# Optimization experiments

Hardware: AMD Instinct MI355X
Metric: run time of the kernel (lower is better)

Reference implementation:

```python
import jax, jax.numpy as jnp
import numpy as np

B, S, DM, NH, DK, DFF = 4, 2048, 512, 8, 64, 2048
EPS = 1e-5


def setup_inputs() -> dict:
    key = jax.random.key(0)
    ks = jax.random.split(key, 16)
    sd = 1.0 / np.sqrt(DM)
    inp = {
        'x': jax.random.normal(ks[0], (B, S, DM), dtype=jnp.float32),
        'wq': jax.random.normal(ks[1], (DM, DM), dtype=jnp.float32) * sd,
        'bq': jnp.zeros((DM,), dtype=jnp.float32),
        'wk': jax.random.normal(ks[2], (DM, DM), dtype=jnp.float32) * sd,
        'bk': jnp.zeros((DM,), dtype=jnp.float32),
        'wv': jax.random.normal(ks[3], (DM, DM), dtype=jnp.float32) * sd,
        'bv': jnp.zeros((DM,), dtype=jnp.float32),
        'wo': jax.random.normal(ks[4], (DM, DM), dtype=jnp.float32) * sd,
        'bo': jnp.zeros((DM,), dtype=jnp.float32),
        'ln_g': jnp.ones((DM,), dtype=jnp.float32),
        'ln_b': jnp.zeros((DM,), dtype=jnp.float32),
        'w1': jax.random.normal(ks[5], (DFF, DM), dtype=jnp.float32) * sd,
        'b1': jnp.zeros((DFF,), dtype=jnp.float32),
        'w2': jax.random.normal(ks[6], (DM, DFF), dtype=jnp.float32) * (1.0 / np.sqrt(DFF)),
        'b2': jnp.zeros((DM,), dtype=jnp.float32),
    }
    return inp


def _layernorm(x, g, b):
    mu = jnp.mean(x, axis=-1, keepdims=True)
    var = jnp.mean(jnp.square(x - mu), axis=-1, keepdims=True)
    return (x - mu) * jax.lax.rsqrt(var + EPS) * g + b


def reference(x, wq, bq, wk, bk, wv, bv, wo, bo, ln_g, ln_b, w1, b1, w2, b2):
    # projections (torch Linear: y = x @ W.T + b)
    q = x @ wq.T + bq
    k = x @ wk.T + bk
    v = x @ wv.T + bv
    # chunk along feature dim into NH heads of size DK
    q = q.reshape(B, S, NH, DK)
    k = k.reshape(B, S, NH, DK)
    v = v.reshape(B, S, NH, DK)
    scores = jnp.einsum('bihd,bjhd->bhij', q, k) / np.sqrt(DK)  # [B,NH,S,S]
    probs = jax.nn.softmax(scores, axis=-1)
    o = jnp.einsum('bhij,bjhd->bihd', probs, v).reshape(B, S, DM)
    o = o @ wo.T + bo
    # residual + shared layernorm (dropout p=0 -> identity)
    h = _layernorm(o + x, ln_g, ln_b)
    ff = jax.nn.relu(h @ w1.T + b1) @ w2.T + b2
    return _layernorm(ff + h, ln_g, ln_b)
```

## Files before the change

### kernel.cpp

```cpp
#include <hip/hip_runtime.h>

typedef __attribute__((ext_vector_type(8))) short short8;
typedef __attribute__((ext_vector_type(8))) unsigned short ushort8;
typedef __attribute__((ext_vector_type(4))) unsigned short ushort4v;
typedef __attribute__((ext_vector_type(4))) float f32x4;
typedef __attribute__((ext_vector_type(16))) float f32x16;

#define DEV static __device__ __forceinline__

DEV unsigned short f2bf(float f) {
  unsigned u = __builtin_bit_cast(unsigned, f);
  u += 0x7fffu + ((u >> 16) & 1u);
  return (unsigned short)(u >> 16);
}

DEV float bf2f(unsigned short u) {
  return __builtin_bit_cast(float, (unsigned)u << 16);
}

DEV void gload_lds16(const void* g, void* l) {
  __builtin_amdgcn_global_load_lds((__attribute__((address_space(1))) void*)g,
                                   (__attribute__((address_space(3))) void*)l,
                                   16, 0, 0);
}

DEV unsigned cvtpk(float lo, float hi) {
  unsigned u;
  asm("v_cvt_pk_bf16_f32 %0, %1, %2" : "=v"(u) : "v"(lo), "v"(hi));
  return u;
}

DEV short8 pack4(unsigned a, unsigned b, unsigned c, unsigned d) {
  int4 t = make_int4((int)a, (int)b, (int)c, (int)d);
  return __builtin_bit_cast(short8, t);
}

__global__ __launch_bounds__(256) void cvt_all_k(
    const float4* __restrict__ wq, const float4* __restrict__ wk,
    const float4* __restrict__ wv, const float4* __restrict__ wo,
    const float4* __restrict__ w1, const float4* __restrict__ w2,
    const float4* __restrict__ x, ushort4v* __restrict__ wqkv,
    ushort4v* __restrict__ wob, ushort4v* __restrict__ w1b,
    ushort4v* __restrict__ w2b, ushort4v* __restrict__ xb) {
  const int i = threadIdx.x;
  const int b = blockIdx.x;
  const float4* s;
  ushort4v* d;
  size_t u;
  if (b < 256)       { s = wq; d = wqkv;          u = (size_t)b * 256 + i; }
  else if (b < 512)  { s = wk; d = wqkv + 65536;  u = (size_t)(b - 256) * 256 + i; }
  else if (b < 768)  { s = wv; d = wqkv + 131072; u = (size_t)(b - 512) * 256 + i; }
  else if (b < 1024) { s = wo; d = wob;           u = (size_t)(b - 768) * 256 + i; }
  else if (b < 2048) { s = w1; d = w1b;           u = (size_t)(b - 1024) * 256 + i; }
  else if (b < 3072) { s = w2; d = w2b;           u = (size_t)(b - 2048) * 256 + i; }
  else               { s = x;  d = xb;            u = (size_t)(b - 3072) * 256 + i; }
  float4 v = s[u];
  ushort4v o = { f2bf(v.x), f2bf(v.y), f2bf(v.z), f2bf(v.w) };
  d[u] = o;
}

__global__ void pack_bias_k(const float* __restrict__ bq, const float* __restrict__ bk,
                            const float* __restrict__ bv, float* __restrict__ o) {
  int i = threadIdx.x;
  o[i] = bq[i];
  o[512 + i] = bk[i];
  o[1024 + i] = bv[i];
}

template <int EPI>
__global__ __launch_bounds__(256) void gemm_bt(
    const unsigned short* __restrict__ A, const unsigned short* __restrict__ Bw,
    const float* __restrict__ bias, int M, int N, int K,
    unsigned short* __restrict__ outb, float* __restrict__ outf,
    const unsigned short* __restrict__ residb) {
  __shared__ __align__(16) unsigned short As[128 * 64];
  __shared__ __align__(16) unsigned short Bs[128 * 64];
  const int tid = threadIdx.x;
  const int lane = tid & 63;
  const int wv = tid >> 6;
  const int wr = wv >> 1, wc = wv & 1;
  const int lrow = lane & 15, lgrp = lane >> 4;
  const int bm = blockIdx.x * 128;
  const int bn = blockIdx.y * 128;

  f32x4 acc[4][4];
#pragma unroll
  for (int m = 0; m < 4; m++)
#pragma unroll
    for (int n = 0; n < 4; n++) acc[m][n] = (f32x4){0.f, 0.f, 0.f, 0.f};

  for (int k0 = 0; k0 < K; k0 += 64) {
    __syncthreads();
#pragma unroll
    for (int i = 0; i < 4; i++) {
      const int sb = wv * 64 + i * 256;
      const int slot = sb + lane;
      const int row = slot >> 3;
      const int cc = (slot & 7) ^ (row & 7);
      gload_lds16(A + (size_t)(bm + row) * K + k0 + cc * 8, &As[sb * 8]);
      gload_lds16(Bw + (size_t)(bn + row) * K + k0 + cc * 8, &Bs[sb * 8]);
    }
    __syncthreads();

#pragma unroll
    for (int kk = 0; kk < 2; kk++) {
      short8 af[4], bfr[4];
#pragma unroll
      for (int m = 0; m < 4; m++) {
        const int row = wr * 64 + m * 16 + lrow;
        af[m] = *(const short8*)&As[row * 64 + (((lgrp + 4 * kk) ^ (row & 7)) * 8)];
      }
#pragma unroll
      for (int n = 0; n < 4; n++) {
        const int row = wc * 64 + n * 16 + lrow;
        bfr[n] = *(const short8*)&Bs[row * 64 + (((lgrp + 4 * kk) ^ (row & 7)) * 8)];
      }
#pragma unroll
      for (int m = 0; m < 4; m++)
#pragma unroll
        for (int n = 0; n < 4; n++)
          acc[m][n] = __builtin_amdgcn_mfma_f32_16x16x32_bf16(af[m], bfr[n], acc[m][n], 0, 0, 0);
    }
  }

  if constexpr (EPI == 0) {
    const int proj = bn >> 9;
    if (proj == 2) {
      __shared__ __align__(16) unsigned short VT[128 * 136];
#pragma unroll
      for (int n = 0; n < 4; n++) {
        const int cl = wc * 64 + n * 16 + lrow;
        const float bval = bias[bn + cl];
#pragma unroll
        for (int m = 0; m < 4; m++)
#pragma unroll
          for (int r = 0; r < 4; r++)
            VT[cl * 136 + wr * 64 + m * 16 + lgrp * 4 + r] = f2bf(acc[m][n][r] + bval);
      }
      __syncthreads();
      const int j = (bn - 1024) >> 7;
      const int b = bm >> 11;
      const int sbase = bm & 2047;
      unsigned short* vout = outb + (size_t)2 * 4194304;
#pragma unroll
      for (int q = 0; q < 8; q++) {
        const int chunk = q * 256 + tid;
        const int cl = chunk >> 4, s8 = chunk & 15;
        const int head = 2 * j + (cl >> 6), d = cl & 63;
        ushort8 val = *(const ushort8*)&VT[cl * 136 + s8 * 8];
        *(ushort8*)(vout + ((size_t)(b * 8 + head) * 64 + d) * 2048 + sbase + s8 * 8) = val;
      }
    } else {
      const float qs = (proj == 0) ? 0.18033688011f : 1.0f;
#pragma unroll
      for (int m = 0; m < 4; m++) {
#pragma unroll
        for (int n = 0; n < 4; n++) {
          const int gcol = bn + wc * 64 + n * 16 + lrow;
          const float bval = bias[gcol];
          const int feat = gcol & 511;
          const int head = feat >> 6, d = feat & 63;
#pragma unroll
          for (int r = 0; r < 4; r++) {
            const int grow = bm + wr * 64 + m * 16 + lgrp * 4 + r;
            const int b = grow >> 11, s = grow & 2047;
            const int bh = b * 8 + head;
            outb[(size_t)proj * 4194304 + ((size_t)bh * 2048 + s) * 64 + d] =
                f2bf((acc[m][n][r] + bval) * qs);
          }
        }
      }
    }
  } else {
#pragma unroll
    for (int m = 0; m < 4; m++) {
#pragma unroll
      for (int n = 0; n < 4; n++) {
        const int gcol = bn + wc * 64 + n * 16 + lrow;
        const float bval = bias[gcol];
#pragma unroll
        for (int r = 0; r < 4; r++) {
          const int grow = bm + wr * 64 + m * 16 + lgrp * 4 + r;
          float v = acc[m][n][r] + bval;
          const size_t o = (size_t)grow * N + gcol;
          if constexpr (EPI == 1) {
            outb[o] = f2bf(v + bf2f(residb[o]));
          } else if constexpr (EPI == 2) {
            outb[o] = f2bf(v > 0.f ? v : 0.f);
          } else {
            outf[o] = v + bf2f(residb[o]);
          }
        }
      }
    }
  }
}

template <int EPI>
__global__ __launch_bounds__(256) void gemm_n64(
    const unsigned short* __restrict__ A, const unsigned short* __restrict__ Bw,
    const float* __restrict__ bias, int M, int N, int K,
    unsigned short* __restrict__ outb, float* __restrict__ outf,
    const unsigned short* __restrict__ residb) {
  __shared__ __align__(16) unsigned short As[128 * 64];
  __shared__ __align__(16) unsigned short Bs[64 * 64];
  const int tid = threadIdx.x;
  const int lane = tid & 63;
  const int wv = tid >> 6;
  const int lrow = lane & 15, lgrp = lane >> 4;
  const int bm = blockIdx.x * 128;
  const int bn = blockIdx.y * 64;

  f32x4 acc[2][4];
#pragma unroll
  for (int m = 0; m < 2; m++)
#pragma unroll
    for (int n = 0; n < 4; n++) acc[m][n] = (f32x4){0.f, 0.f, 0.f, 0.f};

  for (int k0 = 0; k0 < K; k0 += 64) {
    __syncthreads();
#pragma unroll
    for (int i = 0; i < 4; i++) {
      const int sb = wv * 64 + i * 256;
      const int slot = sb + lane;
      const int row = slot >> 3;
      const int cc = (slot & 7) ^ (row & 7);
      gload_lds16(A + (size_t)(bm + row) * K + k0 + cc * 8, &As[sb * 8]);
    }
#pragma unroll
    for (int i = 0; i < 2; i++) {
      const int sb = wv * 64 + i * 256;
      const int slot = sb + lane;
      const int row = slot >> 3;
      const int cc = (slot & 7) ^ (row & 7);
      gload_lds16(Bw + (size_t)(bn + row) * K + k0 + cc * 8, &Bs[sb * 8]);
    }
    __syncthreads();

#pragma unroll
    for (int kk = 0; kk < 2; kk++) {
      short8 af[2], bfr[4];
#pragma unroll
      for (int m = 0; m < 2; m++) {
        const int row = wv * 32 + m * 16 + lrow;
        af[m] = *(const short8*)&As[row * 64 + (((lgrp + 4 * kk) ^ (row & 7)) * 8)];
      }
#pragma unroll
      for (int n = 0; n < 4; n++) {
        const int row = n * 16 + lrow;
        bfr[n] = *(const short8*)&Bs[row * 64 + (((lgrp + 4 * kk) ^ (row & 7)) * 8)];
      }
#pragma unroll
      for (int m = 0; m < 2; m++)
#pragma unroll
        for (int n = 0; n < 4; n++)
          acc[m][n] = __builtin_amdgcn_mfma_f32_16x16x32_bf16(af[m], bfr[n], acc[m][n], 0, 0, 0);
    }
  }

#pragma unroll
  for (int m = 0; m < 2; m++) {
#pragma unroll
    for (int n = 0; n < 4; n++) {
      const int gcol = bn + n * 16 + lrow;
      const float bval = bias[gcol];
#pragma unroll
      for (int r = 0; r < 4; r++) {
        const int grow = bm + wv * 32 + m * 16 + lgrp * 4 + r;
        float v = acc[m][n][r] + bval;
        const size_t o = (size_t)grow * N + gcol;
        if constexpr (EPI == 1) {
          outb[o] = f2bf(v + bf2f(residb[o]));
        } else {
          outf[o] = v + bf2f(residb[o]);
        }
      }
    }
  }
}

__global__ __launch_bounds__(256) void attn_k(
    const unsigned short* __restrict__ Qg, const unsigned short* __restrict__ Kg,
    const unsigned short* __restrict__ Vg, unsigned short* __restrict__ Og) {
  __shared__ __align__(16) unsigned short Kl[64 * 64];
  __shared__ __align__(16) unsigned short Vl[64 * 64];
  const int tid = threadIdx.x, lane = tid & 63, wq = tid >> 6;
  const int ql = lane & 31;
  const int hi = lane >> 5;
  const int bid = blockIdx.x;
  const int lin = (bid & 7) * 64 + (bid >> 3);
  const int bh = lin >> 4;
  const int q0 = (lin & 15) * 128;
  const int qw = q0 + wq * 32;
  const size_t hbase = (size_t)bh * (2048 * 64);

  short8 qreg[4];
  {
    const unsigned short* qp = Qg + hbase + (size_t)(qw + ql) * 64 + hi * 8;
#pragma unroll
    for (int i = 0; i < 4; i++) qreg[i] = *(const short8*)(qp + 16 * i);
  }

  f32x16 oac0 = {0.f, 0.f, 0.f, 0.f, 0.f, 0.f, 0.f, 0.f,
                 0.f, 0.f, 0.f, 0.f, 0.f, 0.f, 0.f, 0.f};
  f32x16 oac1 = oac0;
  float lr = 0.f;

  for (int kt = 0; kt < 2048; kt += 64) {
    __syncthreads();
#pragma unroll
    for (int i = 0; i < 2; i++) {
      const int sb = wq * 64 + i * 256;
      const int slot = sb + lane;
      const int r = slot >> 3;
      const int c = (slot & 7) ^ (r & 7);
      gload_lds16(Kg + hbase + (size_t)(kt + r) * 64 + c * 8, &Kl[sb * 8]);
      gload_lds16(Vg + hbase + (size_t)r * 2048 + kt + c * 8, &Vl[sb * 8]);
    }
    __syncthreads();

    f32x16 sc0 = {0.f, 0.f, 0.f, 0.f, 0.f, 0.f, 0.f, 0.f,
                  0.f, 0.f, 0.f, 0.f, 0.f, 0.f, 0.f, 0.f};
    f32x16 sc1 = sc0;
    __builtin_amdgcn_s_setprio(1);
#pragma unroll
    for (int i = 0; i < 4; i++) {
      const int c8 = 2 * i + hi;
      const int r0 = ql;
      const int r1 = ql + 32;
      short8 ka = *(const short8*)&Kl[(r0 * 8 + (c8 ^ (r0 & 7))) * 8];
      short8 kb = *(const short8*)&Kl[(r1 * 8 + (c8 ^ (r1 & 7))) * 8];
      sc0 = __builtin_amdgcn_mfma_f32_32x32x16_bf16(ka, qreg[i], sc0, 0, 0, 0);
      sc1 = __builtin_amdgcn_mfma_f32_32x32x16_bf16(kb, qreg[i], sc1, 0, 0, 0);
    }
    __builtin_amdgcn_s_setprio(0);

    short8 pa[4];
#pragma unroll
    for (int t2 = 0; t2 < 2; t2++) {
      const f32x16& sc = t2 ? sc1 : sc0;
      float p[16];
#pragma unroll
      for (int r = 0; r < 16; r++) {
        p[r] = __builtin_amdgcn_exp2f(sc[r]);
        lr += p[r];
      }
      unsigned w0a = cvtpk(p[0], p[1]),  w0b = cvtpk(p[2], p[3]);
      unsigned w1a = cvtpk(p[4], p[5]),  w1b = cvtpk(p[6], p[7]);
      unsigned w2a = cvtpk(p[8], p[9]),  w2b = cvtpk(p[10], p[11]);
      unsigned w3a = cvtpk(p[12], p[13]), w3b = cvtpk(p[14], p[15]);
      unsigned ea = hi ? w0a : w1a, eb = hi ? w0b : w1b;
      unsigned ra = (unsigned)__shfl_xor((int)ea, 32);
      unsigned rb = (unsigned)__shfl_xor((int)eb, 32);
      pa[2 * t2] = hi ? pack4(ra, rb, w1a, w1b) : pack4(w0a, w0b, ra, rb);
      ea = hi ? w2a : w3a; eb = hi ? w2b : w3b;
      ra = (unsigned)__shfl_xor((int)ea, 32);
      rb = (unsigned)__shfl_xor((int)eb, 32);
      pa[2 * t2 + 1] = hi ? pack4(ra, rb, w3a, w3b) : pack4(w2a, w2b, ra, rb);
    }

    __builtin_amdgcn_s_setprio(1);
#pragma unroll
    for (int ks = 0; ks < 4; ks++) {
      const int c8 = 2 * ks + hi;
      const int r0 = ql;
      const int r1 = ql + 32;
      short8 vb0 = *(const short8*)&Vl[(r0 * 8 + (c8 ^ (r0 & 7))) * 8];
      short8 vb1 = *(const short8*)&Vl[(r1 * 8 + (c8 ^ (r1 & 7))) * 8];
      oac0 = __builtin_amdgcn_mfma_f32_32x32x16_bf16(pa[ks], vb0, oac0, 0, 0, 0);
      oac1 = __builtin_amdgcn_mfma_f32_32x32x16_bf16(pa[ks], vb1, oac1, 0, 0, 0);
    }
    __builtin_amdgcn_s_setprio(0);
  }

  lr += __shfl_xor(lr, 32);
  const float inv = 1.0f / lr;

  const int b = bh >> 3, h = bh & 7;
#pragma unroll
  for (int r = 0; r < 16; r++) {
    const int qrow = (r & 3) + 8 * (r >> 2) + 4 * hi;
    const float invr = __shfl(inv, qrow);
    const size_t base = ((size_t)(b * 2048 + qw + qrow)) * 512 + h * 64 + ql;
    Og[base] = f2bf(oac0[r] * invr);
    Og[base + 32] = f2bf(oac1[r] * invr);
  }
}

__global__ __launch_bounds__(64) void ln_k(const float* __restrict__ in,
                                           const float* __restrict__ g,
                                           const float* __restrict__ bb,
                                           float* __restrict__ outf) {
  const int row = blockIdx.x, lane = threadIdx.x;
  const float4* p = (const float4*)(in + (size_t)row * 512);
  float4 a = p[lane], b4 = p[lane + 64];
  float s = a.x + a.y + a.z + a.w + b4.x + b4.y + b4.z + b4.w;
#pragma unroll
  for (int off = 32; off >= 1; off >>= 1) s += __shfl_xor(s, off);
  const float mu = s * (1.f / 512.f);
  float q = 0.f;
  {
    float d;
    d = a.x - mu; q += d * d; d = a.y - mu; q += d * d;
    d = a.z - mu; q += d * d; d = a.w - mu; q += d * d;
    d = b4.x - mu; q += d * d; d = b4.y - mu; q += d * d;
    d = b4.z - mu; q += d * d; d = b4.w - mu; q += d * d;
  }
#pragma unroll
  for (int off = 32; off >= 1; off >>= 1) q += __shfl_xor(q, off);
  const float rstd = rsqrtf(q * (1.f / 512.f) + 1e-5f);
  const float4* gp = (const float4*)g;
  const float4* bp = (const float4*)bb;
  float4 g0 = gp[lane], g1 = gp[lane + 64], c0 = bp[lane], c1 = bp[lane + 64];
  float4 o0, o1;
  o0.x = (a.x - mu) * rstd * g0.x + c0.x;
  o0.y = (a.y - mu) * rstd * g0.y + c0.y;
  o0.z = (a.z - mu) * rstd * g0.z + c0.z;
  o0.w = (a.w - mu) * rstd * g0.w + c0.w;
  o1.x = (b4.x - mu) * rstd * g1.x + c1.x;
  o1.y = (b4.y - mu) * rstd * g1.y + c1.y;
  o1.z = (b4.z - mu) * rstd * g1.z + c1.z;
  o1.w = (b4.w - mu) * rstd * g1.w + c1.w;
  float4* of = (float4*)(outf + (size_t)row * 512);
  of[lane] = o0;
  of[lane + 64] = o1;
}

__global__ __launch_bounds__(64) void ln_bf_k(const unsigned short* __restrict__ in,
                                              const float* __restrict__ g,
                                              const float* __restrict__ bb,
                                              unsigned short* __restrict__ out) {
  const int row = blockIdx.x, lane = threadIdx.x;
  ushort8 v = *(const ushort8*)(in + (size_t)row * 512 + lane * 8);
  float f[8];
#pragma unroll
  for (int j = 0; j < 8; j++) f[j] = bf2f(v[j]);
  float s = 0.f;
#pragma unroll
  for (int j = 0; j < 8; j++) s += f[j];
#pragma unroll
  for (int off = 32; off >= 1; off >>= 1) s += __shfl_xor(s, off);
  const float mu = s * (1.f / 512.f);
  float q = 0.f;
#pragma unroll
  for (int j = 0; j < 8; j++) { const float d = f[j] - mu; q += d * d; }
#pragma unroll
  for (int off = 32; off >= 1; off >>= 1) q += __shfl_xor(q, off);
  const float rstd = rsqrtf(q * (1.f / 512.f) + 1e-5f);
  const float4* gp = (const float4*)g;
  const float4* bp = (const float4*)bb;
  float4 g0 = gp[lane * 2], g1 = gp[lane * 2 + 1];
  float4 c0 = bp[lane * 2], c1 = bp[lane * 2 + 1];
  const float gg[8] = {g0.x, g0.y, g0.z, g0.w, g1.x, g1.y, g1.z, g1.w};
  const float cc[8] = {c0.x, c0.y, c0.z, c0.w, c1.x, c1.y, c1.z, c1.w};
  ushort8 ov;
#pragma unroll
  for (int j = 0; j < 8; j++) ov[j] = f2bf((f[j] - mu) * rstd * gg[j] + cc[j]);
  *(ushort8*)(out + (size_t)row * 512 + lane * 8) = ov;
}

extern "C" void kernel_launch(void* const* d_in, const int* in_sizes, int n_in,
                              void* d_out, int out_size, void* d_ws, size_t ws_size,
                              hipStream_t stream) {
  const float* x = (const float*)d_in[0];
  const float* wq = (const float*)d_in[1];
  const float* bq = (const float*)d_in[2];
  const float* wk = (const float*)d_in[3];
  const float* bk = (const float*)d_in[4];
  const float* wv = (const float*)d_in[5];
  const float* bv = (const float*)d_in[6];
  const float* wo = (const float*)d_in[7];
  const float* bo = (const float*)d_in[8];
  const float* ln_g = (const float*)d_in[9];
  const float* ln_b = (const float*)d_in[10];
  const float* w1 = (const float*)d_in[11];
  const float* b1 = (const float*)d_in[12];
  const float* w2 = (const float*)d_in[13];
  const float* b2 = (const float*)d_in[14];

  unsigned short* ws_u = (unsigned short*)d_ws;
  unsigned short* wqkv = ws_u;
  unsigned short* wob = wqkv + 786432;
  unsigned short* w1b = wob + 262144;
  unsigned short* w2b = w1b + 1048576;
  unsigned short* xb = w2b + 1048576;
  unsigned short* qb = xb + 4194304;
  unsigned short* kb = qb + 4194304;
  unsigned short* vtb = kb + 4194304;
  unsigned short* ob = vtb + 4194304;
  unsigned short* s1b = ob + 4194304;
  unsigned short* hb = s1b + 4194304;
  unsigned short* f1b = qb;
  float* bqkv = (float*)(hb + 4194304);

  cvt_all_k<<<7168, 256, 0, stream>>>(
      (const float4*)wq, (const float4*)wk, (const float4*)wv, (const float4*)wo,
      (const float4*)w1, (const float4*)w2, (const float4*)x,
      (ushort4v*)wqkv, (ushort4v*)wob, (ushort4v*)w1b, (ushort4v*)w2b,
      (ushort4v*)xb);
  pack_bias_k<<<1, 512, 0, stream>>>(bq, bk, bv, bqkv);

  gemm_bt<0><<<dim3(64, 12), 256, 0, stream>>>(xb, wqkv, bqkv, 8192, 1536, 512,
                                               qb, nullptr, nullptr);
  attn_k<<<512, 256, 0, stream>>>(qb, kb, vtb, ob);
  gemm_n64<1><<<dim3(64, 8), 256, 0, stream>>>(ob, wob, bo, 8192, 512, 512,
                                               s1b, nullptr, xb);
  ln_bf_k<<<8192, 64, 0, stream>>>(s1b, ln_g, ln_b, hb);
  gemm_bt<2><<<dim3(64, 16), 256, 0, stream>>>(hb, w1b, b1, 8192, 2048, 512,
                                               f1b, nullptr, nullptr);
  gemm_n64<3><<<dim3(64, 8), 256, 0, stream>>>(f1b, w2b, b2, 8192, 512, 2048,
                                               nullptr, (float*)d_out, hb);
  ln_k<<<8192, 64, 0, stream>>>((float*)d_out, ln_g, ln_b, (float*)d_out);
}
```

Measured before the change: 171.7 us.

## Double-buffer K/V tiles in attention and use permlane32 swap for P repack

The attention kernel now keeps two LDS buffers for K and V and issues the async global-to-LDS loads for the next tile before computing on the current one. This cuts the loop down to one barrier per iteration and overlaps the loads with the MFMA and exp work. The P-matrix repacking also swaps the select-plus-__shfl_xor exchange for v_permlane32_swap instructions. The cost is doubled LDS use per block, and correctness depends on the end-of-iteration barrier also covering completion of the async loads.

```diff
diff --git a/kernel.cpp b/kernel.cpp
--- a/kernel.cpp
+++ b/kernel.cpp
@@ -28,6 +28,10 @@
   unsigned u;
   asm("v_cvt_pk_bf16_f32 %0, %1, %2" : "=v"(u) : "v"(lo), "v"(hi));
   return u;
+}
+
+DEV void pl32(unsigned& a, unsigned& b) {
+  asm("v_permlane32_swap_b32 %0, %1" : "+v"(a), "+v"(b));
 }
 
 DEV short8 pack4(unsigned a, unsigned b, unsigned c, unsigned d) {
@@ -282,8 +286,8 @@
 __global__ __launch_bounds__(256) void attn_k(
     const unsigned short* __restrict__ Qg, const unsigned short* __restrict__ Kg,
     const unsigned short* __restrict__ Vg, unsigned short* __restrict__ Og) {
-  __shared__ __align__(16) unsigned short Kl[64 * 64];
-  __shared__ __align__(16) unsigned short Vl[64 * 64];
+  __shared__ __align__(16) unsigned short Kl[2][64 * 64];
+  __shared__ __align__(16) unsigned short Vl[2][64 * 64];
   const int tid = threadIdx.x, lane = tid & 63, wq = tid >> 6;
   const int ql = lane & 31;
   const int hi = lane >> 5;
@@ -294,6 +298,10 @@
   const int qw = q0 + wq * 32;
   const size_t hbase = (size_t)bh * (2048 * 64);
 
+  const int sb0 = wq * 64, sb1 = wq * 64 + 256;
+  const int r0s = (sb0 + lane) >> 3, c0s = ((sb0 + lane) & 7) ^ (r0s & 7);
+  const int r1s = (sb1 + lane) >> 3, c1s = ((sb1 + lane) & 7) ^ (r1s & 7);
+
   short8 qreg[4];
   {
     const unsigned short* qp = Qg + hbase + (size_t)(qw + ql) * 64 + hi * 8;
@@ -306,18 +314,22 @@
   f32x16 oac1 = oac0;
   float lr = 0.f;
 
-  for (int kt = 0; kt < 2048; kt += 64) {
-    __syncthreads();
-#pragma unroll
-    for (int i = 0; i < 2; i++) {
-      const int sb = wq * 64 + i * 256;
-      const int slot = sb + lane;
-      const int r = slot >> 3;
-      const int c = (slot & 7) ^ (r & 7);
-      gload_lds16(Kg + hbase + (size_t)(kt + r) * 64 + c * 8, &Kl[sb * 8]);
-      gload_lds16(Vg + hbase + (size_t)r * 2048 + kt + c * 8, &Vl[sb * 8]);
-    }
-    __syncthreads();
+  gload_lds16(Kg + hbase + (size_t)r0s * 64 + c0s * 8, &Kl[0][sb0 * 8]);
+  gload_lds16(Vg + hbase + (size_t)r0s * 2048 + c0s * 8, &Vl[0][sb0 * 8]);
+  gload_lds16(Kg + hbase + (size_t)r1s * 64 + c1s * 8, &Kl[0][sb1 * 8]);
+  gload_lds16(Vg + hbase + (size_t)r1s * 2048 + c1s * 8, &Vl[0][sb1 * 8]);
+  __syncthreads();
+
+  for (int it = 0; it < 32; ++it) {
+    const int cur = it & 1;
+    if (it < 31) {
+      const int kt = (it + 1) * 64;
+      const int nxt = cur ^ 1;
+      gload_lds16(Kg + hbase + (size_t)(kt + r0s) * 64 + c0s * 8, &Kl[nxt][sb0 * 8]);
+      gload_lds16(Vg + hbase + (size_t)r0s * 2048 + kt + c0s * 8, &Vl[nxt][sb0 * 8]);
+      gload_lds16(Kg + hbase + (size_t)(kt + r1s) * 64 + c1s * 8, &Kl[nxt][sb1 * 8]);
+      gload_lds16(Vg + hbase + (size_t)r1s * 2048 + kt + c1s * 8, &Vl[nxt][sb1 * 8]);
+    }
 
     f32x16 sc0 = {0.f, 0.f, 0.f, 0.f, 0.f, 0.f, 0.f, 0.f,
                   0.f, 0.f, 0.f, 0.f, 0.f, 0.f, 0.f, 0.f};
@@ -328,8 +340,8 @@
       const int c8 = 2 * i + hi;
       const int r0 = ql;
       const int r1 = ql + 32;
-      short8 ka = *(const short8*)&Kl[(r0 * 8 + (c8 ^ (r0 & 7))) * 8];
-      short8 kb = *(const short8*)&Kl[(r1 * 8 + (c8 ^ (r1 & 7))) * 8];
+      short8 ka = *(const short8*)&Kl[cur][(r0 * 8 + (c8 ^ (r0 & 7))) * 8];
+      short8 kb = *(const short8*)&Kl[cur][(r1 * 8 + (c8 ^ (r1 & 7))) * 8];
       sc0 = __builtin_amdgcn_mfma_f32_32x32x16_bf16(ka, qreg[i], sc0, 0, 0, 0);
       sc1 = __builtin_amdgcn_mfma_f32_32x32x16_bf16(kb, qreg[i], sc1, 0, 0, 0);
     }
@@ -345,18 +357,16 @@
         p[r] = __builtin_amdgcn_exp2f(sc[r]);
         lr += p[r];
       }
-      unsigned w0a = cvtpk(p[0], p[1]),  w0b = cvtpk(p[2], p[3]);
-      unsigned w1a = cvtpk(p[4], p[5]),  w1b = cvtpk(p[6], p[7]);
-      unsigned w2a = cvtpk(p[8], p[9]),  w2b = cvtpk(p[10], p[11]);
+      unsigned w0a = cvtpk(p[0], p[1]),   w0b = cvtpk(p[2], p[3]);
+      unsigned w1a = cvtpk(p[4], p[5]),   w1b = cvtpk(p[6], p[7]);
+      unsigned w2a = cvtpk(p[8], p[9]),   w2b = cvtpk(p[10], p[11]);
       unsigned w3a = cvtpk(p[12], p[13]), w3b = cvtpk(p[14], p[15]);
-      unsigned ea = hi ? w0a : w1a, eb = hi ? w0b : w1b;
-      unsigned ra = (unsigned)__shfl_xor((int)ea, 32);
-      unsigned rb = (unsigned)__shfl_xor((int)eb, 32);
-      pa[2 * t2] = hi ? pack4(ra, rb, w1a, w1b) : pack4(w0a, w0b, ra, rb);
-      ea = hi ? w2a : w3a; eb = hi ? w2b : w3b;
-      ra = (unsigned)__shfl_xor((int)ea, 32);
-      rb = (unsigned)__shfl_xor((int)eb, 32);
-      pa[2 * t2 + 1] = hi ? pack4(ra, rb, w3a, w3b) : pack4(w2a, w2b, ra, rb);
+      pl32(w0a, w1a);
+      pl32(w0b, w1b);
+      pa[2 * t2] = pack4(w0a, w0b, w1a, w1b);
+      pl32(w2a, w3a);
+      pl32(w2b, w3b);
+      pa[2 * t2 + 1] = pack4(w2a, w2b, w3a, w3b);
     }
 
     __builtin_amdgcn_s_setprio(1);
@@ -365,12 +375,14 @@
       const int c8 = 2 * ks + hi;
       const int r0 = ql;
       const int r1 = ql + 32;
-      short8 vb0 = *(const short8*)&Vl[(r0 * 8 + (c8 ^ (r0 & 7))) * 8];
-      short8 vb1 = *(const short8*)&Vl[(r1 * 8 + (c8 ^ (r1 & 7))) * 8];
+      short8 vb0 = *(const short8*)&Vl[cur][(r0 * 8 + (c8 ^ (r0 & 7))) * 8];
+      short8 vb1 = *(const short8*)&Vl[cur][(r1 * 8 + (c8 ^ (r1 & 7))) * 8];
       oac0 = __builtin_amdgcn_mfma_f32_32x32x16_bf16(pa[ks], vb0, oac0, 0, 0, 0);
       oac1 = __builtin_amdgcn_mfma_f32_32x32x16_bf16(pa[ks], vb1, oac1, 0, 0, 0);
     }
     __builtin_amdgcn_s_setprio(0);
+
+    __syncthreads();
   }
 
   lr += __shfl_xor(lr, 32);
```

Result: no change. 170.7 us (-0.5%).
